# Performance work log

Hardware: AMD Instinct MI355X
Metric: run time of the kernel (lower is better)

The kernel has to match this reference:

```python
import jax, jax.numpy as jnp
import numpy as np

HOP = 160
FFT = 1024
NUM_LABELS = 72
B, T = 4, 240000


def setup_inputs() -> dict:
    key = jax.random.key(0)
    k1, _ = jax.random.split(key)
    lbl = jax.random.randint(k1, (B, T), 0, NUM_LABELS, dtype=jnp.int64 if jax.config.jax_enable_x64 else jnp.int32)
    weight = jnp.ones((FFT,), dtype=jnp.float32)  # frozen all-ones conv kernel
    return {"lbl": lbl, "weight": weight}


def reference(lbl, weight):
    pad = FFT // 2
    # ReflectionPad1d on the label stream: [B, T] -> [B, L], L = T + 2*pad
    x = jnp.pad(lbl, ((0, 0), (pad, pad)), mode="reflect")
    L = x.shape[-1]
    # one-hot scatter: [B, NUM_LABELS, L] fp32 (dominant memory traffic)
    onehot = jax.nn.one_hot(x, NUM_LABELS, axis=1, dtype=jnp.float32)
    # sliding-window sum of size FFT, stride HOP, per label channel.
    # Conv2d(1,1,(1,FFT),stride=(1,HOP)) over [B,1,C,L] == 1D conv applied to each
    # (batch, label) row independently: fold C into the batch dim.
    y = jax.lax.conv_general_dilated(
        onehot.reshape(B * NUM_LABELS, 1, L),
        weight.reshape(1, 1, FFT),
        window_strides=(HOP,),
        padding="VALID",
        dimension_numbers=("NCH", "OIH", "NCH"),
    )  # [B*C, 1, n_out]
    n_out = y.shape[-1]
    counts = y.reshape(B, NUM_LABELS, n_out)
    # majority label per window
    return jnp.argmax(counts, axis=1)
```

## Files before the change

### kernel.cpp

```cpp
#include <hip/hip_runtime.h>

#define HOP 160
#define FFT 1024
#define PAD (FFT / 2)
#define NUM_LABELS 72
#define BATCH 4
#define T 240000
#define NOUT 1501

__global__ __launch_bounds__(256) void label_window_argmax(
    const int* __restrict__ lbl, int* __restrict__ out)
{
    __shared__ int hist[4][NUM_LABELS];
    __shared__ int keys[NUM_LABELS];

    const int tid  = threadIdx.x;
    const int wave = tid >> 6;

    for (int i = tid; i < 4 * NUM_LABELS; i += 256)
        ((int*)hist)[i] = 0;
    __syncthreads();

    const int w = blockIdx.x;
    const int b = blockIdx.y;
    const int* __restrict__ row = lbl + b * T;
    const int start = w * HOP - PAD;

#pragma unroll
    for (int k = 0; k < FFT / 256; ++k) {
        int j = start + tid + k * 256;
        j = (j < 0) ? -j : j;
        j = (j >= T) ? (2 * (T - 1) - j) : j;
        const int lab = row[j];
        atomicAdd(&hist[wave][lab], 1);
    }
    __syncthreads();

    if (tid < NUM_LABELS) {
        const int tot = hist[0][tid] + hist[1][tid] + hist[2][tid] + hist[3][tid];
        keys[tid] = (tot << 7) | (NUM_LABELS - 1 - tid);
    }
    __syncthreads();

    if (tid == 0) {
        int best = keys[0];
#pragma unroll
        for (int i = 1; i < NUM_LABELS; ++i)
            best = max(best, keys[i]);
        out[b * NOUT + w] = NUM_LABELS - 1 - (best & 127);
    }
}

extern "C" void kernel_launch(void* const* d_in, const int* in_sizes, int n_in,
                              void* d_out, int out_size, void* d_ws, size_t ws_size,
                              hipStream_t stream) {
    const int* lbl = (const int*)d_in[0];
    int* out = (int*)d_out;

    dim3 grid(NOUT, BATCH);
    label_window_argmax<<<grid, 256, 0, stream>>>(lbl, out);
}
```

Baseline: 61.98 us.

## Process multiple windows per block with sliding histogram updates and wave-shuffle argmax

Each block now computes R=8 consecutive output windows, building the first histogram fully and then updating it incrementally by removing the HOP labels leaving the window and adding the HOP labels entering. The serial 72-element argmax in one thread is replaced by a wave-level shuffle max reduction. This cuts redundant loads and LDS atomics, but serializes the windows within a block, adding barriers per step and reducing the number of blocks in flight.

```diff
diff --git a/kernel.cpp b/kernel.cpp
--- a/kernel.cpp
+++ b/kernel.cpp
@@ -7,6 +7,8 @@
 #define BATCH 4
 #define T 240000
 #define NOUT 1501
+#define R 8
+#define NBLK ((NOUT + R - 1) / R)
 
 __global__ __launch_bounds__(256) void label_window_argmax(
     const int* __restrict__ lbl, int* __restrict__ out)
@@ -16,38 +18,66 @@
 
     const int tid  = threadIdx.x;
     const int wave = tid >> 6;
+    const int lane = tid & 63;
 
     for (int i = tid; i < 4 * NUM_LABELS; i += 256)
         ((int*)hist)[i] = 0;
+
+    const int b  = blockIdx.y;
+    const int w0 = blockIdx.x * R;
+    const int* __restrict__ row = lbl + b * T;
+
+    auto refl = [&](int j) {
+        j = (j < 0) ? -j : j;
+        j = (j >= T) ? (2 * (T - 1) - j) : j;
+        return j;
+    };
+
     __syncthreads();
 
-    const int w = blockIdx.x;
-    const int b = blockIdx.y;
-    const int* __restrict__ row = lbl + b * T;
-    const int start = w * HOP - PAD;
+    {
+        const int s = w0 * HOP - PAD;
+#pragma unroll
+        for (int k = 0; k < 4; ++k) {
+            const int lab = row[refl(s + tid + k * 256)];
+            atomicAdd(&hist[wave][lab], 1);
+        }
+    }
 
+    for (int step = 0; step < R; ++step) {
+        const int w = w0 + step;
+        if (w >= NOUT) break;
+        __syncthreads();
+
+        if (tid < NUM_LABELS) {
+            const int tot = hist[0][tid] + hist[1][tid] + hist[2][tid] + hist[3][tid];
+            keys[tid] = (tot << 7) | (NUM_LABELS - 1 - tid);
+        }
+        __syncthreads();
+
+        if (wave == 0) {
+            int k = keys[lane];
+            if (lane < NUM_LABELS - 64)
+                k = max(k, keys[64 + lane]);
 #pragma unroll
-    for (int k = 0; k < FFT / 256; ++k) {
-        int j = start + tid + k * 256;
-        j = (j < 0) ? -j : j;
-        j = (j >= T) ? (2 * (T - 1) - j) : j;
-        const int lab = row[j];
-        atomicAdd(&hist[wave][lab], 1);
-    }
-    __syncthreads();
+            for (int off = 32; off; off >>= 1)
+                k = max(k, __shfl_xor(k, off, 64));
+            if (lane == 0)
+                out[b * NOUT + w] = NUM_LABELS - 1 - (k & 127);
+        }
 
-    if (tid < NUM_LABELS) {
-        const int tot = hist[0][tid] + hist[1][tid] + hist[2][tid] + hist[3][tid];
-        keys[tid] = (tot << 7) | (NUM_LABELS - 1 - tid);
-    }
-    __syncthreads();
-
-    if (tid == 0) {
-        int best = keys[0];
-#pragma unroll
-        for (int i = 1; i < NUM_LABELS; ++i)
-            best = max(best, keys[i]);
-        out[b * NOUT + w] = NUM_LABELS - 1 - (best & 127);
+        if (step + 1 < R && w + 1 < NOUT) {
+            const int s = w * HOP - PAD;
+            if (tid < HOP) {
+                const int lab = row[refl(s + tid)];
+                atomicAdd(&hist[wave][lab], -1);
+            }
+            const int t2 = tid - (256 - HOP);
+            if (t2 >= 0) {
+                const int lab = row[refl(s + FFT + t2)];
+                atomicAdd(&hist[wave][lab], 1);
+            }
+        }
     }
 }
 
@@ -57,6 +87,6 @@
     const int* lbl = (const int*)d_in[0];
     int* out = (int*)d_out;
 
-    dim3 grid(NOUT, BATCH);
+    dim3 grid(NBLK, BATCH);
     label_window_argmax<<<grid, 256, 0, stream>>>(lbl, out);
 }
```

Result: no change. 61.23 us (-1.2%).
